# Optimization experiments

Hardware: AMD Instinct MI355X
Metric: run time of the kernel (lower is better)

## Reference

```python
import jax, jax.numpy as jnp
import numpy as np

B, T, C, H = 2, 4096, 1024, 16
D = C // H
SEGMENTS = ((512, 1), (1024, 2), (2048, 4))  # (segment_length w, dilation r) per LongNet config


def setup_inputs() -> dict:
    key = jax.random.key(0)
    ks = jax.random.split(key, 12)
    s = 0.02
    return {
        "x": jax.random.normal(ks[0], (B, T, C), jnp.float32),
        # outer fused qkv projection (c_attn), stored as [in, out] so y = x @ W + b
        "c_attn_w": jax.random.normal(ks[1], (C, 3 * C), jnp.float32) * s,
        "c_attn_b": jnp.zeros((3 * C,), jnp.float32),
        # inner torchscale MultiheadAttention projections
        "q_w": jax.random.normal(ks[2], (C, C), jnp.float32) * s,
        "q_b": jnp.zeros((C,), jnp.float32),
        "k_w": jax.random.normal(ks[3], (C, C), jnp.float32) * s,
        "k_b": jnp.zeros((C,), jnp.float32),
        "v_w": jax.random.normal(ks[4], (C, C), jnp.float32) * s,
        "v_b": jnp.zeros((C,), jnp.float32),
        "o_w": jax.random.normal(ks[5], (C, C), jnp.float32) * s,
        "o_b": jnp.zeros((C,), jnp.float32),
    }


def _branch(q, k, v, w, r):
    """One dilated-attention branch: segment length w, dilation r.
    q,k,v: [B,H,T,D] (q pre-scaled). Heads use offset = head % r (LongNet).
    Returns (out_full [B,H,T,D], lse_full [B,H,T]) scattered back to full positions.
    """
    b, h_, t, d = q.shape
    n_seg, eff = t // w, w // r
    h = jnp.arange(h_)
    idx = (h % r)[:, None] + jnp.arange(eff)[None, :] * r            # [H, eff] within-segment indices
    pos = jnp.arange(n_seg)[None, :, None] * w + idx[:, None, :]     # [H, n_seg, eff] absolute positions
    hh = h[:, None, None]
    qg = q[:, hh, pos]                                               # [B,H,n_seg,eff,D]
    kg = k[:, hh, pos]
    vg = v[:, hh, pos]
    scores = jnp.einsum('bhsid,bhsjd->bhsij', qg, kg)
    causal = jnp.tril(jnp.ones((eff, eff), bool))                    # order preserved under strided subsampling
    scores = jnp.where(causal, scores, jnp.finfo(scores.dtype).min)
    m = scores.max(-1, keepdims=True)
    p = jnp.exp(scores - m)
    s = p.sum(-1, keepdims=True)
    o = jnp.einsum('bhsij,bhsjd->bhsid', p, vg) / s
    lse = m[..., 0] + jnp.log(s[..., 0])                             # [B,H,n_seg,eff]
    out_full = jnp.zeros((b, h_, t, d), q.dtype).at[:, hh, pos].set(o)
    lse_full = jnp.full((b, h_, t), -1e30, q.dtype).at[:, hh, pos].set(lse)
    return out_full, lse_full


def _forward(x, c_attn_w, c_attn_b, q_w, q_b, k_w, k_b, v_w, v_b, o_w, o_b):
    b, t, c = x.shape
    qkv = x @ c_attn_w + c_attn_b
    qx, kx, vx = jnp.split(qkv, 3, axis=-1)
    q = (qx @ q_w + q_b).reshape(b, t, H, D).transpose(0, 2, 1, 3) * (D ** -0.5)
    k = (kx @ k_w + k_b).reshape(b, t, H, D).transpose(0, 2, 1, 3)
    v = (vx @ v_w + v_b).reshape(b, t, H, D).transpose(0, 2, 1, 3)
    outs, lses = zip(*[_branch(q, k, v, w, r) for w, r in SEGMENTS])
    O = jnp.stack(outs)                                              # [S,B,H,T,D]
    L = jnp.stack(lses)                                              # [S,B,H,T]
    # LongNet combination: weight each branch by its softmax denominator (via lse)
    m = L.max(0)
    wts = jnp.exp(L - m)                                             # [S,B,H,T]
    y = (wts[..., None] * O).sum(0) / wts.sum(0)[..., None]          # [B,H,T,D]
    y = y.transpose(0, 2, 1, 3).reshape(b, t, c)
    return y @ o_w + o_b


def reference(x, c_attn_w, c_attn_b, q_w, q_b, k_w, k_b, v_w, v_b, o_w, o_b):
    return _forward(x, c_attn_w, c_attn_b, q_w, q_b, k_w, k_b, v_w, v_b, o_w, o_b)
```

## Files before the change

### kernel.cpp

```cpp
#include <hip/hip_runtime.h>
#include <hip/hip_bf16.h>

typedef __bf16 bf16x8 __attribute__((ext_vector_type(8)));
typedef float  f32x4  __attribute__((ext_vector_type(4)));

__device__ __forceinline__ unsigned short f2bf(float f) {
    union { float f; unsigned int u; } v; v.f = f;
    return (unsigned short)((v.u + 0x8000u) >> 16);
}
__device__ __forceinline__ float bf2f(unsigned short h) {
    union { unsigned int u; float f; } v; v.u = ((unsigned int)h) << 16;
    return v.f;
}

typedef __attribute__((address_space(3))) unsigned int lds_u32_t;
typedef const __attribute__((address_space(1))) unsigned int glb_u32_t;
__device__ __forceinline__ void gl_lds16(const void* g, void* l) {
    __builtin_amdgcn_global_load_lds((glb_u32_t*)g, (lds_u32_t*)l, 16, 0, 0);
}

__global__ void k_cast(const float* __restrict__ in, unsigned short* __restrict__ out, int n) {
    int i = (blockIdx.x * blockDim.x + threadIdx.x) * 4;
    if (i + 3 < n) {
        float4 v = *reinterpret_cast<const float4*>(in + i);
        ushort4 o;
        o.x = f2bf(v.x); o.y = f2bf(v.y); o.z = f2bf(v.z); o.w = f2bf(v.w);
        *reinterpret_cast<ushort4*>(out + i) = o;
    }
}

__global__ void k_transpose4(const float* __restrict__ s0, const float* __restrict__ s1,
                             const float* __restrict__ s2, const float* __restrict__ s3,
                             unsigned short* __restrict__ d0, unsigned short* __restrict__ d1,
                             unsigned short* __restrict__ d2, unsigned short* __restrict__ d3) {
    __shared__ float tile[32][33];
    int z = blockIdx.z;
    const float* in = (z == 0) ? s0 : (z == 1) ? s1 : (z == 2) ? s2 : s3;
    unsigned short* out = (z == 0) ? d0 : (z == 1) ? d1 : (z == 2) ? d2 : d3;
    int n0 = blockIdx.x * 32, k0 = blockIdx.y * 32;
    int tx = threadIdx.x, ty = threadIdx.y;
    #pragma unroll
    for (int i = 0; i < 4; ++i)
        tile[ty + i * 8][tx] = in[(size_t)(k0 + ty + i * 8) * 1024 + n0 + tx];
    __syncthreads();
    #pragma unroll
    for (int i = 0; i < 4; ++i)
        out[(size_t)(n0 + ty + i * 8) * 1024 + k0 + tx] = f2bf(tile[tx][ty + i * 8]);
}

__global__ __launch_bounds__(256) void k_gemm(
    const unsigned short* __restrict__ A, int lda,
    const unsigned short* __restrict__ Bt, int ldb,
    const float* __restrict__ bias,
    void* __restrict__ out,
    int M, int N, int K, int mode, float scale)
{
    __shared__ unsigned short As[128 * 32];
    __shared__ unsigned short Bs[128 * 32];
    int tid  = threadIdx.x;
    int lane = tid & 63, wv = tid >> 6;
    int quad = lane >> 4, l16 = lane & 15;
    int bm = blockIdx.y * 128, bn = blockIdx.x * 128;
    int wm = (wv >> 1) * 64,  wn = (wv & 1) * 64;

    f32x4 acc[4][4] = {};
    int srow = tid >> 2, scol = (tid & 3) * 8;

    for (int k0 = 0; k0 < K; k0 += 32) {
        #pragma unroll
        for (int s = 0; s < 2; ++s) {
            int row = s * 64 + srow;
            gl_lds16(&A[(size_t)(bm + row) * lda + k0 + scol], &As[(s * 256 + wv * 64) * 8]);
            gl_lds16(&Bt[(size_t)(bn + row) * ldb + k0 + scol], &Bs[(s * 256 + wv * 64) * 8]);
        }
        __syncthreads();
        bf16x8 af[4], bfv[4];
        #pragma unroll
        for (int mi = 0; mi < 4; ++mi)
            af[mi] = *reinterpret_cast<const bf16x8*>(&As[(wm + mi * 16 + l16) * 32 + quad * 8]);
        #pragma unroll
        for (int ni = 0; ni < 4; ++ni)
            bfv[ni] = *reinterpret_cast<const bf16x8*>(&Bs[(wn + ni * 16 + l16) * 32 + quad * 8]);
        #pragma unroll
        for (int mi = 0; mi < 4; ++mi)
            #pragma unroll
            for (int ni = 0; ni < 4; ++ni)
                acc[mi][ni] = __builtin_amdgcn_mfma_f32_16x16x32_bf16(af[mi], bfv[ni], acc[mi][ni], 0, 0, 0);
        __syncthreads();
    }

    #pragma unroll
    for (int mi = 0; mi < 4; ++mi) {
        #pragma unroll
        for (int ni = 0; ni < 4; ++ni) {
            int col = bn + wn + ni * 16 + l16;
            float bsv = bias[col];
            #pragma unroll
            for (int ri = 0; ri < 4; ++ri) {
                int row = bm + wm + mi * 16 + quad * 4 + ri;
                float val = (acc[mi][ni][ri] + bsv) * scale;
                if (mode == 0)
                    reinterpret_cast<unsigned short*>(out)[(size_t)row * N + col] = f2bf(val);
                else
                    reinterpret_cast<float*>(out)[(size_t)row * N + col] = val;
            }
        }
    }
}

__global__ __launch_bounds__(256) void k_foldw(
    const unsigned short* __restrict__ wT3,
    const unsigned short* __restrict__ WcB,
    unsigned short* __restrict__ Weff)
{
    __shared__ unsigned short As[128 * 32];
    __shared__ unsigned short Bs[128 * 32];
    int z = blockIdx.z;
    const unsigned short* A  = wT3 + (size_t)z * 1024 * 1024;
    const unsigned short* Bt = WcB + z * 1024;
    unsigned short* out = Weff + (size_t)z * 1024 * 1024;
    float scale = (z == 0) ? 0.1803368801f : 1.f;

    int tid  = threadIdx.x;
    int lane = tid & 63, wv = tid >> 6;
    int quad = lane >> 4, l16 = lane & 15;
    int bm = blockIdx.y * 128, bn = blockIdx.x * 128;
    int wm = (wv >> 1) * 64,  wn = (wv & 1) * 64;

    f32x4 acc[4][4] = {};
    int srow = tid >> 2, scol = (tid & 3) * 8;

    for (int k0 = 0; k0 < 1024; k0 += 32) {
        #pragma unroll
        for (int s = 0; s < 2; ++s) {
            int row = s * 64 + srow;
            gl_lds16(&A[(size_t)(bm + row) * 1024 + k0 + scol], &As[(s * 256 + wv * 64) * 8]);
            gl_lds16(&Bt[(size_t)(bn + row) * 3072 + k0 + scol], &Bs[(s * 256 + wv * 64) * 8]);
        }
        __syncthreads();
        bf16x8 af[4], bfv[4];
        #pragma unroll
        for (int mi = 0; mi < 4; ++mi)
            af[mi] = *reinterpret_cast<const bf16x8*>(&As[(wm + mi * 16 + l16) * 32 + quad * 8]);
        #pragma unroll
        for (int ni = 0; ni < 4; ++ni)
            bfv[ni] = *reinterpret_cast<const bf16x8*>(&Bs[(wn + ni * 16 + l16) * 32 + quad * 8]);
        #pragma unroll
        for (int mi = 0; mi < 4; ++mi)
            #pragma unroll
            for (int ni = 0; ni < 4; ++ni)
                acc[mi][ni] = __builtin_amdgcn_mfma_f32_16x16x32_bf16(af[mi], bfv[ni], acc[mi][ni], 0, 0, 0);
        __syncthreads();
    }

    #pragma unroll
    for (int mi = 0; mi < 4; ++mi)
        #pragma unroll
        for (int ni = 0; ni < 4; ++ni) {
            int col = bn + wn + ni * 16 + l16;
            #pragma unroll
            for (int ri = 0; ri < 4; ++ri) {
                int row = bm + wm + mi * 16 + quad * 4 + ri;
                out[(size_t)row * 1024 + col] = f2bf(acc[mi][ni][ri] * scale);
            }
        }
}

__global__ void k_foldb(const unsigned short* __restrict__ wT3, const float* __restrict__ bc,
                        const float* __restrict__ qb, const float* __restrict__ kb,
                        const float* __restrict__ vb, float* __restrict__ beff)
{
    int id = blockIdx.x * blockDim.x + threadIdx.x;
    int z = id >> 10, n = id & 1023;
    const unsigned short* row = wT3 + (size_t)z * 1024 * 1024 + (size_t)n * 1024;
    const float* b2 = (z == 0) ? qb : (z == 1) ? kb : vb;
    float s = 0.f;
    for (int c = 0; c < 1024; ++c) s += bc[z * 1024 + c] * bf2f(row[c]);
    s += b2[n];
    if (z == 0) s *= 0.1803368801f;
    beff[id] = s;
}

__global__ __launch_bounds__(256) void k_gemm3(
    const unsigned short* __restrict__ A,
    const unsigned short* __restrict__ Weff,
    const float* __restrict__ beff,
    unsigned short* __restrict__ Qg, unsigned short* __restrict__ Kg,
    unsigned short* __restrict__ Vtg)
{
    __shared__ unsigned short smem[8320];
    unsigned short* As = smem;
    unsigned short* Bs = smem + 4096;
    int z = blockIdx.z;
    const unsigned short* Bt = Weff + (size_t)z * 1024 * 1024;
    const float* bias = beff + z * 1024;

    int tid  = threadIdx.x;
    int lane = tid & 63, wv = tid >> 6;
    int quad = lane >> 4, l16 = lane & 15;
    int bm = blockIdx.y * 128, bn = blockIdx.x * 128;
    int wm = (wv >> 1) * 64,  wn = (wv & 1) * 64;

    f32x4 acc[4][4] = {};
    int srow = tid >> 2, scol = (tid & 3) * 8;

    for (int k0 = 0; k0 < 1024; k0 += 32) {
        #pragma unroll
        for (int s = 0; s < 2; ++s) {
            int row = s * 64 + srow;
            gl_lds16(&A[(size_t)(bm + row) * 1024 + k0 + scol], &As[(s * 256 + wv * 64) * 8]);
            gl_lds16(&Bt[(size_t)(bn + row) * 1024 + k0 + scol], &Bs[(s * 256 + wv * 64) * 8]);
        }
        __syncthreads();
        bf16x8 af[4], bfv[4];
        #pragma unroll
        for (int mi = 0; mi < 4; ++mi)
            af[mi] = *reinterpret_cast<const bf16x8*>(&As[(wm + mi * 16 + l16) * 32 + quad * 8]);
        #pragma unroll
        for (int ni = 0; ni < 4; ++ni)
            bfv[ni] = *reinterpret_cast<const bf16x8*>(&Bs[(wn + ni * 16 + l16) * 32 + quad * 8]);
        #pragma unroll
        for (int mi = 0; mi < 4; ++mi)
            #pragma unroll
            for (int ni = 0; ni < 4; ++ni)
                acc[mi][ni] = __builtin_amdgcn_mfma_f32_16x16x32_bf16(af[mi], bfv[ni], acc[mi][ni], 0, 0, 0);
        __syncthreads();
    }

    if (z < 2) {
        unsigned short* dst = (z == 0) ? Qg : Kg;
        #pragma unroll
        for (int mi = 0; mi < 4; ++mi)
            #pragma unroll
            for (int ni = 0; ni < 4; ++ni) {
                int col = bn + wn + ni * 16 + l16;
                float bsv = bias[col];
                int hh = col >> 6, d = col & 63;
                #pragma unroll
                for (int ri = 0; ri < 4; ++ri) {
                    int row = bm + wm + mi * 16 + quad * 4 + ri;
                    unsigned short bv = f2bf(acc[mi][ni][ri] + bsv);
                    int b = row >> 12, t = row & 4095;
                    int bh = b * 16 + hh;
                    { int slot = t >> 9, idx = t & 511;
                      dst[((size_t)(slot * 32 + bh) * 512 + idx) * 64 + d] = bv; }
                    if (((t ^ hh) & 1) == 0) {
                        int slot = 8 + (t >> 10), idx = (t & 1023) >> 1;
                        dst[((size_t)(slot * 32 + bh) * 512 + idx) * 64 + d] = bv;
                    }
                    if (((t ^ hh) & 3) == 0) {
                        int slot = 12 + (t >> 11), idx = (t & 2047) >> 2;
                        dst[((size_t)(slot * 32 + bh) * 512 + idx) * 64 + d] = bv;
                    }
                }
            }
    } else {
        unsigned short* Vt = smem;
        int b = bm >> 12, t0 = bm & 4095;
        #pragma unroll
        for (int half = 0; half < 2; ++half) {
            if ((wn >> 6) == half) {
                #pragma unroll
                for (int mi = 0; mi < 4; ++mi)
                    #pragma unroll
                    for (int ni = 0; ni < 4; ++ni) {
                        int col = bn + wn + ni * 16 + l16;
                        float bsv = bias[col];
                        int din = ni * 16 + l16;
                        #pragma unroll
                        for (int ri = 0; ri < 4; ++ri) {
                            int rowt = wm + mi * 16 + quad * 4 + ri;
                            Vt[din * 130 + rowt] = f2bf(acc[mi][ni][ri] + bsv);
                        }
                    }
            }
            __syncthreads();
            int d = tid >> 2, part = tid & 3;
            int h_glob = (bn >> 6) + half;
            int bh = b * 16 + h_glob;
            const unsigned short* lrow = &Vt[d * 130];
            {
                int slot = t0 >> 9;
                size_t dst = ((size_t)(slot * 32 + bh) * 64 + d) * 512 + (t0 & 511) + part * 32;
                unsigned short buf[32];
                #pragma unroll
                for (int j = 0; j < 32; ++j) buf[j] = lrow[part * 32 + j];
                #pragma unroll
                for (int j = 0; j < 4; ++j)
                    *reinterpret_cast<uint4*>(&Vtg[dst + j * 8]) = reinterpret_cast<const uint4*>(buf)[j];
            }
            {
                int j0 = h_glob & 1;
                int slot = 8 + (t0 >> 10);
                size_t dst = ((size_t)(slot * 32 + bh) * 64 + d) * 512 + ((t0 & 1023) >> 1) + part * 16;
                unsigned short buf[16];
                #pragma unroll
                for (int j = 0; j < 16; ++j) buf[j] = lrow[j0 + 2 * (part * 16 + j)];
                #pragma unroll
                for (int j = 0; j < 2; ++j)
                    *reinterpret_cast<uint4*>(&Vtg[dst + j * 8]) = reinterpret_cast<const uint4*>(buf)[j];
            }
            {
                int j0 = h_glob & 3;
                int slot = 12 + (t0 >> 11);
                size_t dst = ((size_t)(slot * 32 + bh) * 64 + d) * 512 + ((t0 & 2047) >> 2) + part * 8;
                unsigned short buf[8];
                #pragma unroll
                for (int j = 0; j < 8; ++j) buf[j] = lrow[j0 + 4 * (part * 8 + j)];
                *reinterpret_cast<uint4*>(&Vtg[dst]) = *reinterpret_cast<const uint4*>(buf);
            }
            __syncthreads();
        }
    }
}

__global__ __launch_bounds__(256, 3) void k_attn(
    const unsigned short* __restrict__ Qg,
    const unsigned short* __restrict__ Kg,
    const unsigned short* __restrict__ Vtg,
    unsigned short* __restrict__ Og,
    float* __restrict__ Lg)
{
    __shared__ unsigned short Ks[2][64 * 72];
    __shared__ unsigned short Vs[2][64 * 72];

    int tid  = threadIdx.x;
    int lane = tid & 63, wv = tid >> 6;
    int quad = lane >> 4, l16 = lane & 15;
    int q8   = quad << 3;
    int pq = blockIdx.x, ys = blockIdx.y, bh = blockIdx.z;
    int jt_end = 2 * (3 - pq) + 1;
    size_t sb = (size_t)(ys * 32 + bh) * (512 * 64);
    const unsigned short* qp = Qg + sb;
    const unsigned short* kp = Kg + sb;
    const unsigned short* vp = Vtg + sb;
    unsigned short* op = Og + sb;
    float* lp = Lg + (size_t)(ys * 32 + bh) * 512;

    int rw[2] = { pq * 128 + wv * 32, (3 - pq) * 128 + wv * 32 };

    int srow = tid >> 3, sc8 = (tid & 7) * 8;
    int prow = ((srow >> 2) & 1) * 16 + ((srow >> 3) & 3) * 4 + (srow & 3);
    uint4 kr[2], vr[2];
    {
        #pragma unroll
        for (int s = 0; s < 2; ++s) {
            int row = s * 32 + srow;
            kr[s] = *reinterpret_cast<const uint4*>(&kp[(size_t)row * 64 + sc8]);
            vr[s] = *reinterpret_cast<const uint4*>(&vp[(size_t)row * 512 + sc8]);
        }
    }

    bf16x8 qf[2][2][2];
    #pragma unroll
    for (int qi = 0; qi < 2; ++qi)
        #pragma unroll
        for (int m16 = 0; m16 < 2; ++m16)
            #pragma unroll
            for (int kk = 0; kk < 2; ++kk)
                qf[qi][m16][kk] = *reinterpret_cast<const bf16x8*>(
                    &qp[(size_t)(rw[qi] + m16 * 16 + l16) * 64 + kk * 32 + quad * 8]);

    f32x4 acc[2][2][4] = {};
    float l4[2][2] = {};

    for (int jt = 0; jt <= jt_end; ++jt) {
        unsigned short* Kb = &Ks[jt & 1][0];
        unsigned short* Vb = &Vs[jt & 1][0];
        #pragma unroll
        for (int s = 0; s < 2; ++s) {
            *reinterpret_cast<uint4*>(&Kb[(s * 32 + prow) * 72 + sc8]) = kr[s];
            *reinterpret_cast<uint4*>(&Vb[(s * 32 + srow) * 72 + sc8]) = vr[s];
        }
        if (jt < jt_end) {
            #pragma unroll
            for (int s = 0; s < 2; ++s) {
                int row = s * 32 + srow;
                kr[s] = *reinterpret_cast<const uint4*>(&kp[(size_t)((jt + 1) * 64 + row) * 64 + sc8]);
                vr[s] = *reinterpret_cast<const uint4*>(&vp[(size_t)row * 512 + (jt + 1) * 64 + sc8]);
            }
        }
        __syncthreads();

        #pragma unroll
        for (int qi = 0; qi < 2; ++qi) {
            #pragma unroll
            for (int m16 = 0; m16 < 2; ++m16) {
                int rowbase = rw[qi] + m16 * 16;
                if (jt * 64 > rowbase + 15) continue;

                f32x4 sacc[4];
                __builtin_amdgcn_s_setprio(1);
                #pragma unroll
                for (int nt = 0; nt < 4; ++nt) {
                    bf16x8 b0 = *reinterpret_cast<const bf16x8*>(&Kb[(nt * 16 + l16) * 72 + quad * 8]);
                    bf16x8 b1 = *reinterpret_cast<const bf16x8*>(&Kb[(nt * 16 + l16) * 72 + 32 + quad * 8]);
                    f32x4 s4 = {};
                    s4 = __builtin_amdgcn_mfma_f32_16x16x32_bf16(b0, qf[qi][m16][0], s4, 0, 0, 0);
                    s4 = __builtin_amdgcn_mfma_f32_16x16x32_bf16(b1, qf[qi][m16][1], s4, 0, 0, 0);
                    sacc[nt] = s4;
                }
                __builtin_amdgcn_s_setprio(0);

                if (jt * 64 + 63 > rowbase) {
                    int qrow = rowbase + l16;
                    #pragma unroll
                    for (int nt = 0; nt < 4; ++nt)
                        #pragma unroll
                        for (int ri = 0; ri < 4; ++ri) {
                            int kj = jt * 64 + (nt >> 1) * 32 + (nt & 1) * 4 + q8 + ri;
                            if (kj > qrow) sacc[nt][ri] = -1e30f;
                        }
                }
                float ls = 0.f;
                #pragma unroll
                for (int nt = 0; nt < 4; ++nt)
                    #pragma unroll
                    for (int ri = 0; ri < 4; ++ri) {
                        float p = __builtin_amdgcn_exp2f(sacc[nt][ri]);
                        sacc[nt][ri] = p;
                        ls += p;
                    }
                l4[qi][m16] += ls;

                union { unsigned int u[4]; bf16x8 v; } p0u, p1u;
                asm("v_cvt_pk_bf16_f32 %0, %1, %2" : "=v"(p0u.u[0]) : "v"(sacc[0][0]), "v"(sacc[0][1]));
                asm("v_cvt_pk_bf16_f32 %0, %1, %2" : "=v"(p0u.u[1]) : "v"(sacc[0][2]), "v"(sacc[0][3]));
                asm("v_cvt_pk_bf16_f32 %0, %1, %2" : "=v"(p0u.u[2]) : "v"(sacc[1][0]), "v"(sacc[1][1]));
                asm("v_cvt_pk_bf16_f32 %0, %1, %2" : "=v"(p0u.u[3]) : "v"(sacc[1][2]), "v"(sacc[1][3]));
                asm("v_cvt_pk_bf16_f32 %0, %1, %2" : "=v"(p1u.u[0]) : "v"(sacc[2][0]), "v"(sacc[2][1]));
                asm("v_cvt_pk_bf16_f32 %0, %1, %2" : "=v"(p1u.u[1]) : "v"(sacc[2][2]), "v"(sacc[2][3]));
                asm("v_cvt_pk_bf16_f32 %0, %1, %2" : "=v"(p1u.u[2]) : "v"(sacc[3][0]), "v"(sacc[3][1]));
                asm("v_cvt_pk_bf16_f32 %0, %1, %2" : "=v"(p1u.u[3]) : "v"(sacc[3][2]), "v"(sacc[3][3]));

                __builtin_amdgcn_s_setprio(1);
                #pragma unroll
                for (int dt = 0; dt < 4; ++dt) {
                    bf16x8 v0 = *reinterpret_cast<const bf16x8*>(&Vb[(dt * 16 + l16) * 72 + quad * 8]);
                    bf16x8 v1 = *reinterpret_cast<const bf16x8*>(&Vb[(dt * 16 + l16) * 72 + 32 + quad * 8]);
                    f32x4 a4 = acc[qi][m16][dt];
                    a4 = __builtin_amdgcn_mfma_f32_16x16x32_bf16(p0u.v, v0, a4, 0, 0, 0);
                    a4 = __builtin_amdgcn_mfma_f32_16x16x32_bf16(p1u.v, v1, a4, 0, 0, 0);
                    acc[qi][m16][dt] = a4;
                }
                __builtin_amdgcn_s_setprio(0);
            }
        }
    }

    #pragma unroll
    for (int qi = 0; qi < 2; ++qi)
        #pragma unroll
        for (int m16 = 0; m16 < 2; ++m16) {
            int rowb = rw[qi] + m16 * 16;
            float L = l4[qi][m16];
            L += __shfl_xor(L, 16);
            L += __shfl_xor(L, 32);
            float inv[4];
            #pragma unroll
            for (int ri = 0; ri < 4; ++ri)
                inv[ri] = 1.f / __shfl(L, quad * 4 + ri);
            #pragma unroll
            for (int dt = 0; dt < 4; ++dt)
                #pragma unroll
                for (int ri = 0; ri < 4; ++ri) {
                    int row = rowb + quad * 4 + ri;
                    op[(size_t)row * 64 + dt * 16 + l16] = f2bf(acc[qi][m16][dt][ri] * inv[ri]);
                }
            if (lane < 16)
                lp[rowb + l16] = __logf(L);
        }
}

__global__ void k_combine(const unsigned short* __restrict__ Og,
                          const float* __restrict__ Lg,
                          unsigned short* __restrict__ yb)
{
    int g   = blockIdx.x * blockDim.x + threadIdx.x;
    int row = g >> 3;
    int d0  = (g & 7) * 8;
    int bh = row >> 12, t = row & 4095;
    int b = bh >> 4, h = bh & 15;

    int slot0 = t >> 9,         idx0 = t & 511;
    int slot1 = 8 + (t >> 10),  idx1 = (t & 1023) >> 1;
    int slot2 = 12 + (t >> 11), idx2 = (t & 2047) >> 2;
    size_t r0 = (size_t)(slot0 * 32 + bh) * 512 + idx0;
    size_t r1 = (size_t)(slot1 * 32 + bh) * 512 + idx1;
    size_t r2 = (size_t)(slot2 * 32 + bh) * 512 + idx2;
    bool c1 = ((t ^ h) & 1) == 0;
    bool c2 = ((t ^ h) & 3) == 0;

    float L0 = Lg[r0];
    float L1 = c1 ? Lg[r1] : -1e30f;
    float L2 = c2 ? Lg[r2] : -1e30f;
    float m  = fmaxf(L0, fmaxf(L1, L2));
    float w0 = __expf(L0 - m), w1 = __expf(L1 - m), w2 = __expf(L2 - m);
    float inv = 1.f / (w0 + w1 + w2);

    uint4 v0 = *reinterpret_cast<const uint4*>(&Og[r0 * 64 + d0]);
    uint4 v1 = *reinterpret_cast<const uint4*>(&Og[r1 * 64 + d0]);
    uint4 v2 = *reinterpret_cast<const uint4*>(&Og[r2 * 64 + d0]);
    const unsigned short* p0 = reinterpret_cast<const unsigned short*>(&v0);
    const unsigned short* p1 = reinterpret_cast<const unsigned short*>(&v1);
    const unsigned short* p2 = reinterpret_cast<const unsigned short*>(&v2);
    unsigned short o[8];
    #pragma unroll
    for (int u = 0; u < 8; ++u)
        o[u] = f2bf((w0 * bf2f(p0[u]) + w1 * bf2f(p1[u]) + w2 * bf2f(p2[u])) * inv);
    size_t yidx = (((size_t)b * 4096 + t) * 1024) + (size_t)h * 64 + d0;
    *reinterpret_cast<uint4*>(&yb[yidx]) = *reinterpret_cast<const uint4*>(o);
}

extern "C" void kernel_launch(void* const* d_in, const int* in_sizes, int n_in,
                              void* d_out, int out_size, void* d_ws, size_t ws_size,
                              hipStream_t stream)
{
    const float* x        = (const float*)d_in[0];
    const float* c_attn_w = (const float*)d_in[1];
    const float* c_attn_b = (const float*)d_in[2];
    const float* q_w      = (const float*)d_in[3];
    const float* q_b      = (const float*)d_in[4];
    const float* k_w      = (const float*)d_in[5];
    const float* k_b      = (const float*)d_in[6];
    const float* v_w      = (const float*)d_in[7];
    const float* v_b      = (const float*)d_in[8];
    const float* o_w      = (const float*)d_in[9];
    const float* o_b      = (const float*)d_in[10];

    char* ws = (char*)d_ws;
    size_t off = 0;
    auto alloc = [&](size_t bytes) -> char* {
        char* p = ws + off; off += (bytes + 255) & ~(size_t)255; return p;
    };
    const size_t GSZ = 14ull * 32 * 512 * 64;
    unsigned short* xb    = (unsigned short*)alloc(8192ull * 1024 * 2);
    unsigned short* WcB   = (unsigned short*)alloc(1024ull * 3072 * 2);
    unsigned short* wqT   = (unsigned short*)alloc(1024ull * 1024 * 2);
    unsigned short* wkT   = (unsigned short*)alloc(1024ull * 1024 * 2);
    unsigned short* wvT   = (unsigned short*)alloc(1024ull * 1024 * 2);
    unsigned short* woT   = (unsigned short*)alloc(1024ull * 1024 * 2);
    unsigned short* Weff  = (unsigned short*)alloc(3ull * 1024 * 1024 * 2);
    float*          beff  = (float*)alloc(3ull * 1024 * 4);
    unsigned short* Qg    = (unsigned short*)alloc(GSZ * 2);
    unsigned short* Kg    = (unsigned short*)alloc(GSZ * 2);
    unsigned short* Vtg   = (unsigned short*)alloc(GSZ * 2);
    unsigned short* Og    = (unsigned short*)alloc(GSZ * 2);
    float*          Lg    = (float*)alloc(14ull * 32 * 512 * 4);
    unsigned short* yb    = xb;
    (void)wkT; (void)wvT;

    k_cast<<<(8192 * 1024) / 1024, 256, 0, stream>>>(x, xb, 8192 * 1024);
    k_cast<<<(1024 * 3072) / 1024, 256, 0, stream>>>(c_attn_w, WcB, 1024 * 3072);
    k_transpose4<<<dim3(32, 32, 4), dim3(32, 8), 0, stream>>>(q_w, k_w, v_w, o_w, wqT, wkT, wvT, woT);
    k_foldw<<<dim3(8, 8, 3), 256, 0, stream>>>(wqT, WcB, Weff);
    k_foldb<<<12, 256, 0, stream>>>(wqT, c_attn_b, q_b, k_b, v_b, beff);
    k_gemm3<<<dim3(8, 64, 3), 256, 0, stream>>>(xb, Weff, beff, Qg, Kg, Vtg);
    k_attn<<<dim3(2, 14, 32), 256, 0, stream>>>(Qg, Kg, Vtg, Og, Lg);
    k_combine<<<4096, 256, 0, stream>>>(Og, Lg, yb);
    k_gemm<<<dim3(8, 64), 256, 0, stream>>>(yb, 1024, woT, 1024, o_b, d_out, 8192, 1024, 1024, 2, 1.f);
}
```

Measured before the change: 379.1 us.

## Swizzle GEMM block order and vectorize epilogue stores via transposed MFMA operands

Swaps the MFMA A/B operands in the GEMMs so each lane holds four consecutive output columns, which lets the epilogues write bias-added results with ushort4/float4 stores instead of scalar stores. The Q/K scatter into the dilated-segment layouts now writes ushort4 chunks. The V path drops the LDS transpose stage and its barriers, writing directly from registers. An XCD-style block-index swizzle is also added to the GEMM kernels to improve L2 locality across chiplets. The trade-off is that the V stores become narrow, scattered writes rather than the previous coalesced 16-byte rows.

```diff
diff --git a/kernel.cpp b/kernel.cpp
--- a/kernel.cpp
+++ b/kernel.cpp
@@ -60,7 +60,16 @@
     int tid  = threadIdx.x;
     int lane = tid & 63, wv = tid >> 6;
     int quad = lane >> 4, l16 = lane & 15;
-    int bm = blockIdx.y * 128, bn = blockIdx.x * 128;
+
+    int nwg = gridDim.x * gridDim.y;
+    int lin = blockIdx.y * gridDim.x + blockIdx.x;
+    int bx = blockIdx.x, by = blockIdx.y;
+    if ((nwg & 7) == 0) {
+        int swz = (lin & 7) * (nwg >> 3) + (lin >> 3);
+        bx = swz % gridDim.x;
+        by = swz / gridDim.x;
+    }
+    int bm = by * 128, bn = bx * 128;
     int wm = (wv >> 1) * 64,  wn = (wv & 1) * 64;
 
     f32x4 acc[4][4] = {};
@@ -85,24 +94,27 @@
         for (int mi = 0; mi < 4; ++mi)
             #pragma unroll
             for (int ni = 0; ni < 4; ++ni)
-                acc[mi][ni] = __builtin_amdgcn_mfma_f32_16x16x32_bf16(af[mi], bfv[ni], acc[mi][ni], 0, 0, 0);
+                acc[mi][ni] = __builtin_amdgcn_mfma_f32_16x16x32_bf16(bfv[ni], af[mi], acc[mi][ni], 0, 0, 0);
         __syncthreads();
     }
 
     #pragma unroll
     for (int mi = 0; mi < 4; ++mi) {
+        int row = bm + wm + mi * 16 + l16;
         #pragma unroll
         for (int ni = 0; ni < 4; ++ni) {
-            int col = bn + wn + ni * 16 + l16;
-            float bsv = bias[col];
-            #pragma unroll
-            for (int ri = 0; ri < 4; ++ri) {
-                int row = bm + wm + mi * 16 + quad * 4 + ri;
-                float val = (acc[mi][ni][ri] + bsv) * scale;
-                if (mode == 0)
-                    reinterpret_cast<unsigned short*>(out)[(size_t)row * N + col] = f2bf(val);
-                else
-                    reinterpret_cast<float*>(out)[(size_t)row * N + col] = val;
+            int col0 = bn + wn + ni * 16 + quad * 4;
+            float4 b4 = *reinterpret_cast<const float4*>(&bias[col0]);
+            float v0 = (acc[mi][ni][0] + b4.x) * scale;
+            float v1 = (acc[mi][ni][1] + b4.y) * scale;
+            float v2 = (acc[mi][ni][2] + b4.z) * scale;
+            float v3 = (acc[mi][ni][3] + b4.w) * scale;
+            if (mode == 0) {
+                ushort4 o4; o4.x = f2bf(v0); o4.y = f2bf(v1); o4.z = f2bf(v2); o4.w = f2bf(v3);
+                *reinterpret_cast<ushort4*>(&reinterpret_cast<unsigned short*>(out)[(size_t)row * N + col0]) = o4;
+            } else {
+                float4 o4; o4.x = v0; o4.y = v1; o4.z = v2; o4.w = v3;
+                *reinterpret_cast<float4*>(&reinterpret_cast<float*>(out)[(size_t)row * N + col0]) = o4;
             }
         }
     }
@@ -149,21 +161,24 @@
         for (int mi = 0; mi < 4; ++mi)
             #pragma unroll
             for (int ni = 0; ni < 4; ++ni)
-                acc[mi][ni] = __builtin_amdgcn_mfma_f32_16x16x32_bf16(af[mi], bfv[ni], acc[mi][ni], 0, 0, 0);
-        __syncthreads();
-    }
-
-    #pragma unroll
-    for (int mi = 0; mi < 4; ++mi)
+                acc[mi][ni] = __builtin_amdgcn_mfma_f32_16x16x32_bf16(bfv[ni], af[mi], acc[mi][ni], 0, 0, 0);
+        __syncthreads();
+    }
+
+    #pragma unroll
+    for (int mi = 0; mi < 4; ++mi) {
+        int row = bm + wm + mi * 16 + l16;
         #pragma unroll
         for (int ni = 0; ni < 4; ++ni) {
-            int col = bn + wn + ni * 16 + l16;
-            #pragma unroll
-            for (int ri = 0; ri < 4; ++ri) {
-                int row = bm + wm + mi * 16 + quad * 4 + ri;
-                out[(size_t)row * 1024 + col] = f2bf(acc[mi][ni][ri] * scale);
-            }
-        }
+            int col0 = bn + wn + ni * 16 + quad * 4;
+            ushort4 o4;
+            o4.x = f2bf(acc[mi][ni][0] * scale);
+            o4.y = f2bf(acc[mi][ni][1] * scale);
+            o4.z = f2bf(acc[mi][ni][2] * scale);
+            o4.w = f2bf(acc[mi][ni][3] * scale);
+            *reinterpret_cast<ushort4*>(&out[(size_t)row * 1024 + col0]) = o4;
+        }
+    }
 }
 
 __global__ void k_foldb(const unsigned short* __restrict__ wT3, const float* __restrict__ bc,
@@ -188,17 +203,25 @@
     unsigned short* __restrict__ Qg, unsigned short* __restrict__ Kg,
     unsigned short* __restrict__ Vtg)
 {
-    __shared__ unsigned short smem[8320];
-    unsigned short* As = smem;
-    unsigned short* Bs = smem + 4096;
-    int z = blockIdx.z;
-    const unsigned short* Bt = Weff + (size_t)z * 1024 * 1024;
-    const float* bias = beff + z * 1024;
+    __shared__ unsigned short As[128 * 32];
+    __shared__ unsigned short Bs[128 * 32];
 
     int tid  = threadIdx.x;
     int lane = tid & 63, wv = tid >> 6;
     int quad = lane >> 4, l16 = lane & 15;
-    int bm = blockIdx.y * 128, bn = blockIdx.x * 128;
+
+    int nwg = gridDim.x * gridDim.y * gridDim.z;
+    int lin = (blockIdx.z * gridDim.y + blockIdx.y) * gridDim.x + blockIdx.x;
+    int swz = (lin & 7) * (nwg >> 3) + (lin >> 3);
+    int bx  = swz % gridDim.x;
+    int tmp = swz / gridDim.x;
+    int by  = tmp % gridDim.y;
+    int z   = tmp / gridDim.y;
+
+    const unsigned short* Bt = Weff + (size_t)z * 1024 * 1024;
+    const float* bias = beff + z * 1024;
+
+    int bm = by * 128, bn = bx * 128;
     int wm = (wv >> 1) * 64,  wn = (wv & 1) * 64;
 
     f32x4 acc[4][4] = {};
@@ -219,97 +242,86 @@
         #pragma unroll
         for (int ni = 0; ni < 4; ++ni)
             bfv[ni] = *reinterpret_cast<const bf16x8*>(&Bs[(wn + ni * 16 + l16) * 32 + quad * 8]);
-        #pragma unroll
-        for (int mi = 0; mi < 4; ++mi)
-            #pragma unroll
-            for (int ni = 0; ni < 4; ++ni)
-                acc[mi][ni] = __builtin_amdgcn_mfma_f32_16x16x32_bf16(af[mi], bfv[ni], acc[mi][ni], 0, 0, 0);
+        if (z < 2) {
+            #pragma unroll
+            for (int mi = 0; mi < 4; ++mi)
+                #pragma unroll
+                for (int ni = 0; ni < 4; ++ni)
+                    acc[mi][ni] = __builtin_amdgcn_mfma_f32_16x16x32_bf16(bfv[ni], af[mi], acc[mi][ni], 0, 0, 0);
+        } else {
+            #pragma unroll
+            for (int mi = 0; mi < 4; ++mi)
+                #pragma unroll
+                for (int ni = 0; ni < 4; ++ni)
+                    acc[mi][ni] = __builtin_amdgcn_mfma_f32_16x16x32_bf16(af[mi], bfv[ni], acc[mi][ni], 0, 0, 0);
+        }
         __syncthreads();
     }
 
     if (z < 2) {
         unsigned short* dst = (z == 0) ? Qg : Kg;
-        #pragma unroll
-        for (int mi = 0; mi < 4; ++mi)
+        int hh = (bn + wn) >> 6;
+        #pragma unroll
+        for (int mi = 0; mi < 4; ++mi) {
+            int trow = bm + wm + mi * 16 + l16;
+            int b = trow >> 12, t = trow & 4095;
+            int bh = b * 16 + hh;
+            int slot0 = t >> 9,         idx0 = t & 511;
+            int slot1 = 8 + (t >> 10),  idx1 = (t & 1023) >> 1;
+            int slot2 = 12 + (t >> 11), idx2 = (t & 2047) >> 2;
+            bool c1 = ((t ^ hh) & 1) == 0;
+            bool c2 = ((t ^ hh) & 3) == 0;
+            size_t r0 = ((size_t)(slot0 * 32 + bh) * 512 + idx0) * 64;
+            size_t r1 = ((size_t)(slot1 * 32 + bh) * 512 + idx1) * 64;
+            size_t r2 = ((size_t)(slot2 * 32 + bh) * 512 + idx2) * 64;
             #pragma unroll
             for (int ni = 0; ni < 4; ++ni) {
-                int col = bn + wn + ni * 16 + l16;
-                float bsv = bias[col];
-                int hh = col >> 6, d = col & 63;
-                #pragma unroll
-                for (int ri = 0; ri < 4; ++ri) {
-                    int row = bm + wm + mi * 16 + quad * 4 + ri;
-                    unsigned short bv = f2bf(acc[mi][ni][ri] + bsv);
-                    int b = row >> 12, t = row & 4095;
-                    int bh = b * 16 + hh;
-                    { int slot = t >> 9, idx = t & 511;
-                      dst[((size_t)(slot * 32 + bh) * 512 + idx) * 64 + d] = bv; }
-                    if (((t ^ hh) & 1) == 0) {
-                        int slot = 8 + (t >> 10), idx = (t & 1023) >> 1;
-                        dst[((size_t)(slot * 32 + bh) * 512 + idx) * 64 + d] = bv;
-                    }
-                    if (((t ^ hh) & 3) == 0) {
-                        int slot = 12 + (t >> 11), idx = (t & 2047) >> 2;
-                        dst[((size_t)(slot * 32 + bh) * 512 + idx) * 64 + d] = bv;
-                    }
-                }
+                int d0 = ni * 16 + quad * 4;
+                float4 b4 = *reinterpret_cast<const float4*>(&bias[bn + wn + d0]);
+                ushort4 o4;
+                o4.x = f2bf(acc[mi][ni][0] + b4.x);
+                o4.y = f2bf(acc[mi][ni][1] + b4.y);
+                o4.z = f2bf(acc[mi][ni][2] + b4.z);
+                o4.w = f2bf(acc[mi][ni][3] + b4.w);
+                *reinterpret_cast<ushort4*>(&dst[r0 + d0]) = o4;
+                if (c1) *reinterpret_cast<ushort4*>(&dst[r1 + d0]) = o4;
+                if (c2) *reinterpret_cast<ushort4*>(&dst[r2 + d0]) = o4;
             }
+        }
     } else {
-        unsigned short* Vt = smem;
-        int b = bm >> 12, t0 = bm & 4095;
-        #pragma unroll
-        for (int half = 0; half < 2; ++half) {
-            if ((wn >> 6) == half) {
-                #pragma unroll
-                for (int mi = 0; mi < 4; ++mi)
-                    #pragma unroll
-                    for (int ni = 0; ni < 4; ++ni) {
-                        int col = bn + wn + ni * 16 + l16;
-                        float bsv = bias[col];
-                        int din = ni * 16 + l16;
-                        #pragma unroll
-                        for (int ri = 0; ri < 4; ++ri) {
-                            int rowt = wm + mi * 16 + quad * 4 + ri;
-                            Vt[din * 130 + rowt] = f2bf(acc[mi][ni][ri] + bsv);
-                        }
-                    }
+        int h_glob = (bn + wn) >> 6;
+        int j1 = h_glob & 1;
+        int j2 = h_glob & 3;
+        #pragma unroll
+        for (int ni = 0; ni < 4; ++ni) {
+            int d = ni * 16 + l16;
+            float bsv = bias[bn + wn + d];
+            #pragma unroll
+            for (int mi = 0; mi < 4; ++mi) {
+                int t0g = bm + wm + mi * 16 + quad * 4;
+                int b = t0g >> 12, t0 = t0g & 4095;
+                int bh = b * 16 + h_glob;
+                unsigned short val[4];
+                #pragma unroll
+                for (int ri = 0; ri < 4; ++ri) val[ri] = f2bf(acc[mi][ni][ri] + bsv);
+                {
+                    int slot = t0 >> 9;
+                    size_t base = ((size_t)(slot * 32 + bh) * 64 + d) * 512 + (t0 & 511);
+                    *reinterpret_cast<ushort4*>(&Vtg[base]) = *reinterpret_cast<const ushort4*>(val);
+                }
+                {
+                    int slot = 8 + (t0 >> 10);
+                    int idx = ((t0 + j1) & 1023) >> 1;
+                    size_t base = ((size_t)(slot * 32 + bh) * 64 + d) * 512 + idx;
+                    ushort2 o2; o2.x = val[j1]; o2.y = val[j1 + 2];
+                    *reinterpret_cast<ushort2*>(&Vtg[base]) = o2;
+                }
+                {
+                    int slot = 12 + (t0 >> 11);
+                    int idx = ((t0 + j2) & 2047) >> 2;
+                    Vtg[((size_t)(slot * 32 + bh) * 64 + d) * 512 + idx] = val[j2];
+                }
             }
-            __syncthreads();
-            int d = tid >> 2, part = tid & 3;
-            int h_glob = (bn >> 6) + half;
-            int bh = b * 16 + h_glob;
-            const unsigned short* lrow = &Vt[d * 130];
-            {
-                int slot = t0 >> 9;
-                size_t dst = ((size_t)(slot * 32 + bh) * 64 + d) * 512 + (t0 & 511) + part * 32;
-                unsigned short buf[32];
-                #pragma unroll
-                for (int j = 0; j < 32; ++j) buf[j] = lrow[part * 32 + j];
-                #pragma unroll
-                for (int j = 0; j < 4; ++j)
-                    *reinterpret_cast<uint4*>(&Vtg[dst + j * 8]) = reinterpret_cast<const uint4*>(buf)[j];
-            }
-            {
-                int j0 = h_glob & 1;
-                int slot = 8 + (t0 >> 10);
-                size_t dst = ((size_t)(slot * 32 + bh) * 64 + d) * 512 + ((t0 & 1023) >> 1) + part * 16;
-                unsigned short buf[16];
-                #pragma unroll
-                for (int j = 0; j < 16; ++j) buf[j] = lrow[j0 + 2 * (part * 16 + j)];
-                #pragma unroll
-                for (int j = 0; j < 2; ++j)
-                    *reinterpret_cast<uint4*>(&Vtg[dst + j * 8]) = reinterpret_cast<const uint4*>(buf)[j];
-            }
-            {
-                int j0 = h_glob & 3;
-                int slot = 12 + (t0 >> 11);
-                size_t dst = ((size_t)(slot * 32 + bh) * 64 + d) * 512 + ((t0 & 2047) >> 2) + part * 8;
-                unsigned short buf[8];
-                #pragma unroll
-                for (int j = 0; j < 8; ++j) buf[j] = lrow[j0 + 4 * (part * 8 + j)];
-                *reinterpret_cast<uint4*>(&Vtg[dst]) = *reinterpret_cast<const uint4*>(buf);
-            }
-            __syncthreads();
         }
     }
 }
```

Measured after the change: 382.0 us. No clear change (+0.8%).
